# Kernel optimization log

Measured on AMD Instinct MI355X. Metric: run time of the kernel, lower is better.

## Reference

```python
import jax, jax.numpy as jnp
import numpy as np

B, P, D_MODEL = 16, 256, 1024
V, D_LLM = 1000, 4096
H, DK = 16, 64  # d_keys = d_model // n_heads


def setup_inputs() -> dict:
    key = jax.random.key(0)
    ks = jax.random.split(key, 11)
    s = lambda k, shape, fan: jax.random.normal(k, shape, jnp.float32) / np.sqrt(fan)
    return {
        "target_embedding": jax.random.normal(ks[0], (B, P, D_MODEL), jnp.float32),
        "source_embedding": jax.random.normal(ks[1], (V, D_LLM), jnp.float32),
        "value_embedding": jax.random.normal(ks[2], (V, D_LLM), jnp.float32),
        "Wq": s(ks[3], (D_MODEL, H * DK), D_MODEL),
        "bq": jnp.zeros((H * DK,), jnp.float32),
        "Wk": s(ks[4], (D_LLM, H * DK), D_LLM),
        "bk": jnp.zeros((H * DK,), jnp.float32),
        "Wv": s(ks[5], (D_LLM, H * DK), D_LLM),
        "bv": jnp.zeros((H * DK,), jnp.float32),
        "Wo": s(ks[6], (H * DK, D_LLM), H * DK),
        "bo": jnp.zeros((D_LLM,), jnp.float32),
    }


def reference(target_embedding, source_embedding, value_embedding,
              Wq, bq, Wk, bk, Wv, bv, Wo, bo):
    b, p, _ = target_embedding.shape
    v = source_embedding.shape[0]
    # projections
    Q = (target_embedding @ Wq + bq).reshape(b, p, H, DK)   # bphd
    K = (source_embedding @ Wk + bk).reshape(v, H, DK)      # vhd
    Vv = (value_embedding @ Wv + bv).reshape(v, H, DK)      # vhd
    scale = 1.0 / np.sqrt(DK)
    # NOTE: non-standard einsum — contracts over v, elementwise in d
    scores = jnp.einsum('bphd,vhd->bhpd', Q, K)             # [B,H,P,DK]
    A = jax.nn.softmax(scale * scores, axis=-1)             # softmax over head dim d
    # (dropout is identity in eval mode)
    R = jnp.einsum('bhpd,vhd->bphd', A, Vv)                 # A * sum_v V
    out = R.reshape(b, p, H * DK) @ Wo + bo                 # [B,P,D_LLM]
    return out
```

## Files before the change

### kernel.cpp

```cpp
#include <hip/hip_runtime.h>

#define BB   16
#define PP   256
#define BP   4096
#define DMODEL 1024
#define VV   1000
#define DLLM 4096
#define HH   16
#define DK   64
#define HDK  1024

using f32x4 = __attribute__((ext_vector_type(4))) float;
using s16x8 = __attribute__((ext_vector_type(8))) short;
using us8   = __attribute__((ext_vector_type(8))) unsigned short;

__device__ __forceinline__ unsigned short f2bf(float f) {
    unsigned int u = __builtin_bit_cast(unsigned int, f);
    u = (u + 0x7FFFu + ((u >> 16) & 1u)) >> 16;
    return (unsigned short)u;
}

__device__ __forceinline__ void gload_lds16(const unsigned short* g, unsigned short* lds) {
    __builtin_amdgcn_global_load_lds(
        (const __attribute__((address_space(1))) void*)g,
        (__attribute__((address_space(3))) void*)lds,
        16, 0, 0);
}

__device__ __forceinline__ void transpose_body(const float* __restrict__ src,
                                               unsigned short* __restrict__ dst,
                                               int R, int C, int bx, int by, int t,
                                               float (*tile)[33]) {
    int x = t & 7, y = t >> 3;
    int c0 = bx * 32, r0 = by * 32;
    float4 v = *reinterpret_cast<const float4*>(&src[(size_t)(r0 + y) * C + c0 + x * 4]);
    tile[y][x * 4 + 0] = v.x; tile[y][x * 4 + 1] = v.y;
    tile[y][x * 4 + 2] = v.z; tile[y][x * 4 + 3] = v.w;
    __syncthreads();
    ushort4 o = make_ushort4(f2bf(tile[x * 4 + 0][y]), f2bf(tile[x * 4 + 1][y]),
                             f2bf(tile[x * 4 + 2][y]), f2bf(tile[x * 4 + 3][y]));
    *reinterpret_cast<ushort4*>(&dst[(size_t)(c0 + y) * R + r0 + x * 4]) = o;
}

__global__ void mega1(const float* __restrict__ src0, const float* __restrict__ src1,
                      float* __restrict__ part1,
                      const float* __restrict__ target, unsigned short* __restrict__ tgt_bf,
                      const float* __restrict__ Wq, unsigned short* __restrict__ wq_t,
                      const float* __restrict__ Wo, unsigned short* __restrict__ wo_t) {
    __shared__ float tile[32][33];
    int b = blockIdx.x, t = threadIdx.x;
    if (b < 320) {
        int z = b / 160, rem = b % 160, y = rem >> 2, x = rem & 3;
        int col4 = x * 256 + t;
        const float4* src = reinterpret_cast<const float4*>(z ? src1 : src0);
        int r0 = y * 25;
        float4 acc = make_float4(0.f, 0.f, 0.f, 0.f);
        for (int r = 0; r < 25; ++r) {
            float4 v = src[(size_t)(r0 + r) * (DLLM / 4) + col4];
            acc.x += v.x; acc.y += v.y; acc.z += v.z; acc.w += v.w;
        }
        reinterpret_cast<float4*>(part1)[(size_t)(z * 40 + y) * (DLLM / 4) + col4] = acc;
    } else if (b < 320 + 2048) {
        int idx = (b - 320) * 256 + t;
        float4 v0 = reinterpret_cast<const float4*>(target)[idx * 2];
        float4 v1 = reinterpret_cast<const float4*>(target)[idx * 2 + 1];
        us8 o = { f2bf(v0.x), f2bf(v0.y), f2bf(v0.z), f2bf(v0.w),
                  f2bf(v1.x), f2bf(v1.y), f2bf(v1.z), f2bf(v1.w) };
        *reinterpret_cast<us8*>(&tgt_bf[(size_t)idx * 8]) = o;
    } else if (b < 320 + 2048 + 1024) {
        int b2 = b - 2368;
        transpose_body(Wq, wq_t, DMODEL, HDK, b2 & 31, b2 >> 5, t, tile);
    } else {
        int b2 = b - 3392;
        transpose_body(Wo, wo_t, HDK, DLLM, b2 & 127, b2 >> 7, t, tile);
    }
}

__global__ void gemv_partial2(const float* __restrict__ Wk, const float* __restrict__ Wv,
                              const float* __restrict__ part1, float* __restrict__ part2) {
    __shared__ float vec[64];
    int c     = blockIdx.x * 256 + threadIdx.x;
    int chunk = blockIdx.y;
    int z     = blockIdx.z;
    const float* W = z ? Wv : Wk;
    if (threadIdx.x < 64) {
        int r = chunk * 64 + threadIdx.x;
        float a = 0.f;
        for (int p = 0; p < 40; ++p)
            a += part1[(size_t)(z * 40 + p) * DLLM + r];
        vec[threadIdx.x] = a;
    }
    __syncthreads();
    float acc = 0.f;
    int r0 = chunk * 64;
    for (int r = 0; r < 64; ++r)
        acc += vec[r] * W[(size_t)(r0 + r) * HDK + c];
    part2[((z * 64 + chunk) * HDK) + c] = acc;
}

__global__ void gemv_reduce(const float* __restrict__ part,
                            const float* __restrict__ bk, const float* __restrict__ bv,
                            float* __restrict__ kvsum) {
    int idx = blockIdx.x * 256 + threadIdx.x;
    int z = idx >> 10, c = idx & 1023;
    float acc = 0.f;
    for (int ch = 0; ch < 64; ++ch) acc += part[(size_t)(z * 64 + ch) * HDK + c];
    acc += (float)VV * (z ? bv[c] : bk[c]);
    kvsum[idx] = acc;
}

template<int EPI, int BMt, int BNt, int WM, int WN, int BMPX, int NXBN, int BNPX>
__global__ __launch_bounds__(WM * WN * 64, 2)
void gemm_ctd3(const unsigned short* __restrict__ A, const unsigned short* __restrict__ Bt,
               float* __restrict__ C, const float* __restrict__ bias,
               const float* __restrict__ kvsum, unsigned short* __restrict__ R,
               int N, int K) {
    constexpr int WAVES = WM * WN;
    constexpr int Mw = BMt / WM;
    constexpr int M_REP = Mw / 16;
    constexpr int NA = BMt * 32 / (WAVES * 512);
    constexpr int NB = BNt * 32 / (WAVES * 512);
    constexpr int NST = NA + NB;
    static_assert(BNt / WN == 64, "wave col span must be 64");
    static_assert(NA >= 1 && NB >= 1, "staging geometry");

    __shared__ __align__(16) unsigned short Asm[3][BMt * 32];
    __shared__ __align__(16) unsigned short Bsm[3][BNt * 32];

    const int xcd = blockIdx.x & 7, l = blockIdx.x >> 3;
    const int bm = ((xcd / NXBN) * BMPX + (l % BMPX)) * BMt;
    const int bn = ((xcd % NXBN) * BNPX + (l / BMPX)) * BNt;

    const int t = threadIdx.x;
    const int w = t >> 6, lane = t & 63;
    const int wr = w / WN, wc = w % WN;
    const int l15 = lane & 15, kgrp = lane >> 4;

    size_t goffA[NA], goffB[NB];
    int ldsoA[NA], ldsoB[NB];
    {
        int s8 = lane & 7, jj = lane >> 3;
#pragma unroll
        for (int i = 0; i < NA; ++i) {
            int sr = (i * WAVES + w) * 8 + jj;
            int x = s8 ^ (sr & 7);
            goffA[i] = (size_t)(bm + sr * 2 + (x >> 2)) * K + (x & 3) * 8;
            ldsoA[i] = (i * WAVES + w) * 512;
        }
#pragma unroll
        for (int i = 0; i < NB; ++i) {
            int sr = (i * WAVES + w) * 8 + jj;
            int x = s8 ^ (sr & 7);
            goffB[i] = (size_t)(bn + sr * 2 + (x >> 2)) * K + (x & 3) * 8;
            ldsoB[i] = (i * WAVES + w) * 512;
        }
    }
    int ra[M_REP], rb[4];
#pragma unroll
    for (int m = 0; m < M_REP; ++m) {
        int r = wr * Mw + m * 16 + l15;
        int s8 = (kgrp + 4 * (r & 1)) ^ ((r >> 1) & 7);
        ra[m] = (r >> 1) * 64 + s8 * 8;
    }
#pragma unroll
    for (int n = 0; n < 4; ++n) {
        int r = wc * 64 + n * 16 + l15;
        int s8 = (kgrp + 4 * (r & 1)) ^ ((r >> 1) & 7);
        rb[n] = (r >> 1) * 64 + s8 * 8;
    }

    f32x4 acc[M_REP][4] = {};

#define STAGE(t_, b_) do { size_t k0_ = (size_t)(t_) * 32;             \
    _Pragma("unroll")                                                  \
    for (int i_ = 0; i_ < NA; ++i_)                                    \
        gload_lds16(A + goffA[i_] + k0_, &Asm[b_][ldsoA[i_]]);         \
    _Pragma("unroll")                                                  \
    for (int i_ = 0; i_ < NB; ++i_)                                    \
        gload_lds16(Bt + goffB[i_] + k0_, &Bsm[b_][ldsoB[i_]]); } while (0)

#define WAIT_NST() do {                                                 \
    if constexpr (NST == 6) asm volatile("s_waitcnt vmcnt(6)" ::: "memory"); \
    else if constexpr (NST == 4) asm volatile("s_waitcnt vmcnt(4)" ::: "memory"); \
    else if constexpr (NST == 3) asm volatile("s_waitcnt vmcnt(3)" ::: "memory"); \
    else asm volatile("s_waitcnt vmcnt(2)" ::: "memory"); } while (0)

    const int nT = K >> 5;
    STAGE(0, 0); STAGE(1, 1);
    WAIT_NST();
    __builtin_amdgcn_s_barrier();

    int cur = 0;
    for (int tk = 0; tk < nT; ++tk) {
        s16x8 af[M_REP], bfr[4];
#pragma unroll
        for (int m = 0; m < M_REP; ++m)
            af[m] = *reinterpret_cast<const s16x8*>(&Asm[cur][ra[m]]);
#pragma unroll
        for (int n = 0; n < 4; ++n)
            bfr[n] = *reinterpret_cast<const s16x8*>(&Bsm[cur][rb[n]]);
        if (tk + 2 < nT) STAGE(tk + 2, cur == 0 ? 2 : cur - 1);
        __builtin_amdgcn_s_setprio(1);
#pragma unroll
        for (int m = 0; m < M_REP; ++m)
#pragma unroll
            for (int n = 0; n < 4; ++n)
                acc[m][n] = __builtin_amdgcn_mfma_f32_16x16x32_bf16(af[m], bfr[n], acc[m][n], 0, 0, 0);
        __builtin_amdgcn_s_setprio(0);
        if (tk + 2 < nT) {
            WAIT_NST();
        } else if (tk + 1 < nT) {
            asm volatile("s_waitcnt vmcnt(0)" ::: "memory");
        }
        if (tk + 1 < nT) __builtin_amdgcn_s_barrier();
        cur = (cur == 2) ? 0 : cur + 1;
    }
#undef STAGE
#undef WAIT_NST

    if (EPI == 0) {
#pragma unroll
        for (int m = 0; m < M_REP; ++m) {
            int grow = bm + wr * Mw + m * 16 + kgrp * 4;
#pragma unroll
            for (int n = 0; n < 4; ++n) {
                int gcol = bn + wc * 64 + n * 16 + l15;
                float bb = bias[gcol];
#pragma unroll
                for (int j = 0; j < 4; ++j)
                    C[(size_t)(grow + j) * N + gcol] = acc[m][n][j] + bb;
            }
        }
    } else {
        float bqv[4], ksv[4], vsv[4];
#pragma unroll
        for (int n = 0; n < 4; ++n) {
            int col = bn + wc * 64 + n * 16 + l15;
            bqv[n] = bias[col];
            ksv[n] = kvsum[col];
            vsv[n] = kvsum[HDK + col];
        }
#pragma unroll
        for (int m = 0; m < M_REP; ++m) {
            int grow = bm + wr * Mw + m * 16 + kgrp * 4;
#pragma unroll
            for (int j = 0; j < 4; ++j) {
                float x[4];
#pragma unroll
                for (int n = 0; n < 4; ++n)
                    x[n] = 0.125f * (acc[m][n][j] + bqv[n]) * ksv[n];
                float mx = fmaxf(fmaxf(x[0], x[1]), fmaxf(x[2], x[3]));
#pragma unroll
                for (int off = 8; off; off >>= 1) mx = fmaxf(mx, __shfl_xor(mx, off));
                float e[4], s = 0.f;
#pragma unroll
                for (int n = 0; n < 4; ++n) { e[n] = __expf(x[n] - mx); s += e[n]; }
#pragma unroll
                for (int off = 8; off; off >>= 1) s += __shfl_xor(s, off);
                float inv = 1.0f / s;
#pragma unroll
                for (int n = 0; n < 4; ++n) {
                    int col = bn + wc * 64 + n * 16 + l15;
                    R[(size_t)(grow + j) * N + col] = f2bf(e[n] * inv * vsv[n]);
                }
            }
        }
    }
}

extern "C" void kernel_launch(void* const* d_in, const int* in_sizes, int n_in,
                              void* d_out, int out_size, void* d_ws, size_t ws_size,
                              hipStream_t stream) {
    const float* target = (const float*)d_in[0];
    const float* source = (const float*)d_in[1];
    const float* value  = (const float*)d_in[2];
    const float* Wq = (const float*)d_in[3];
    const float* bq = (const float*)d_in[4];
    const float* Wk = (const float*)d_in[5];
    const float* bk = (const float*)d_in[6];
    const float* Wv = (const float*)d_in[7];
    const float* bv = (const float*)d_in[8];
    const float* Wo = (const float*)d_in[9];
    const float* bo = (const float*)d_in[10];
    float* out = (float*)d_out;

    char* ws = (char*)d_ws;
    float*          part1  = (float*)(ws);
    float*          part2  = (float*)(ws + 0x180000);
    float*          kvsum  = (float*)(ws + 0x210000);
    unsigned short* tgt_bf = (unsigned short*)(ws + 0x400000);
    unsigned short* wq_t   = (unsigned short*)(ws + 0xC00000);
    unsigned short* wo_t   = (unsigned short*)(ws + 0xE00000);
    unsigned short* Rb     = (unsigned short*)(ws + 0x1600000);

    mega1<<<7488, 256, 0, stream>>>(source, value, part1, target, tgt_bf, Wq, wq_t, Wo, wo_t);

    gemv_partial2<<<dim3(4, 64, 2), 256, 0, stream>>>(Wk, Wv, part1, part2);
    gemv_reduce<<<8, 256, 0, stream>>>(part2, bk, bv, kvsum);

    gemm_ctd3<1, 64, 128, 2, 2, 16, 2, 4><<<512, 256, 0, stream>>>(
        tgt_bf, wq_t, nullptr, bq, kvsum, Rb, HDK, DMODEL);

    gemm_ctd3<0, 256, 128, 2, 2, 8, 4, 8><<<512, 256, 0, stream>>>(
        Rb, wo_t, out, bo, nullptr, nullptr, DLLM, HDK);
}
```

Before: 93.15 us.

## Restructure GEMM main loop with register double-buffered fragments and 4-stage LDS ring

The GEMM K-loop is unrolled by two and keeps two sets of register fragments, so the LDS reads for the next tile are issued before the MFMAs on the current tile. The LDS ring grows from 3 to 4 buffers, which lets the per-iteration barrier move ahead of the fragment reads. The output GEMM also switches from 256x128 to 128x128 tiles with twice as many blocks, trading more A/B reloads for more parallelism. LDS use per block rises, and this may reduce occupancy.

```diff
diff --git a/kernel.cpp b/kernel.cpp
--- a/kernel.cpp
+++ b/kernel.cpp
@@ -111,7 +111,7 @@
 
 template<int EPI, int BMt, int BNt, int WM, int WN, int BMPX, int NXBN, int BNPX>
 __global__ __launch_bounds__(WM * WN * 64, 2)
-void gemm_ctd3(const unsigned short* __restrict__ A, const unsigned short* __restrict__ Bt,
+void gemm_pipe(const unsigned short* __restrict__ A, const unsigned short* __restrict__ Bt,
                float* __restrict__ C, const float* __restrict__ bias,
                const float* __restrict__ kvsum, unsigned short* __restrict__ R,
                int N, int K) {
@@ -124,8 +124,8 @@
     static_assert(BNt / WN == 64, "wave col span must be 64");
     static_assert(NA >= 1 && NB >= 1, "staging geometry");
 
-    __shared__ __align__(16) unsigned short Asm[3][BMt * 32];
-    __shared__ __align__(16) unsigned short Bsm[3][BNt * 32];
+    __shared__ __align__(16) unsigned short Asm[4][BMt * 32];
+    __shared__ __align__(16) unsigned short Bsm[4][BNt * 32];
 
     const int xcd = blockIdx.x & 7, l = blockIdx.x >> 3;
     const int bm = ((xcd / NXBN) * BMPX + (l % BMPX)) * BMt;
@@ -184,39 +184,53 @@
     else if constexpr (NST == 4) asm volatile("s_waitcnt vmcnt(4)" ::: "memory"); \
     else if constexpr (NST == 3) asm volatile("s_waitcnt vmcnt(3)" ::: "memory"); \
     else asm volatile("s_waitcnt vmcnt(2)" ::: "memory"); } while (0)
+#define WAIT_VM0() asm volatile("s_waitcnt vmcnt(0)" ::: "memory")
+
+#define READF(fa_, fb_, buf_) do {                                      \
+    _Pragma("unroll")                                                   \
+    for (int m_ = 0; m_ < M_REP; ++m_)                                  \
+        fa_[m_] = *reinterpret_cast<const s16x8*>(&Asm[buf_][ra[m_]]);  \
+    _Pragma("unroll")                                                   \
+    for (int n_ = 0; n_ < 4; ++n_)                                      \
+        fb_[n_] = *reinterpret_cast<const s16x8*>(&Bsm[buf_][rb[n_]]); } while (0)
+
+#define MFMAS(fa_, fb_) do {                                            \
+    __builtin_amdgcn_s_setprio(1);                                      \
+    _Pragma("unroll")                                                   \
+    for (int m_ = 0; m_ < M_REP; ++m_)                                  \
+        _Pragma("unroll")                                               \
+        for (int n_ = 0; n_ < 4; ++n_)                                  \
+            acc[m_][n_] = __builtin_amdgcn_mfma_f32_16x16x32_bf16(      \
+                fa_[m_], fb_[n_], acc[m_][n_], 0, 0, 0);                \
+    __builtin_amdgcn_s_setprio(0); } while (0)
 
     const int nT = K >> 5;
+    s16x8 fa0[M_REP], fb0[4], fa1[M_REP], fb1[4];
+
     STAGE(0, 0); STAGE(1, 1);
     WAIT_NST();
     __builtin_amdgcn_s_barrier();
-
-    int cur = 0;
-    for (int tk = 0; tk < nT; ++tk) {
-        s16x8 af[M_REP], bfr[4];
-#pragma unroll
-        for (int m = 0; m < M_REP; ++m)
-            af[m] = *reinterpret_cast<const s16x8*>(&Asm[cur][ra[m]]);
-#pragma unroll
-        for (int n = 0; n < 4; ++n)
-            bfr[n] = *reinterpret_cast<const s16x8*>(&Bsm[cur][rb[n]]);
-        if (tk + 2 < nT) STAGE(tk + 2, cur == 0 ? 2 : cur - 1);
-        __builtin_amdgcn_s_setprio(1);
-#pragma unroll
-        for (int m = 0; m < M_REP; ++m)
-#pragma unroll
-            for (int n = 0; n < 4; ++n)
-                acc[m][n] = __builtin_amdgcn_mfma_f32_16x16x32_bf16(af[m], bfr[n], acc[m][n], 0, 0, 0);
-        __builtin_amdgcn_s_setprio(0);
+    READF(fa0, fb0, 0);
+
+    for (int tk = 0; tk < nT; tk += 2) {
+        if (tk + 2 < nT) { STAGE(tk + 2, (tk + 2) & 3); WAIT_NST(); }
+        else             { WAIT_VM0(); }
+        __builtin_amdgcn_s_barrier();
+        READF(fa1, fb1, (tk + 1) & 3);
+        MFMAS(fa0, fb0);
         if (tk + 2 < nT) {
-            WAIT_NST();
-        } else if (tk + 1 < nT) {
-            asm volatile("s_waitcnt vmcnt(0)" ::: "memory");
-        }
-        if (tk + 1 < nT) __builtin_amdgcn_s_barrier();
-        cur = (cur == 2) ? 0 : cur + 1;
+            if (tk + 3 < nT) { STAGE(tk + 3, (tk + 3) & 3); WAIT_NST(); }
+            else             { WAIT_VM0(); }
+            __builtin_amdgcn_s_barrier();
+            READF(fa0, fb0, (tk + 2) & 3);
+        }
+        MFMAS(fa1, fb1);
     }
 #undef STAGE
 #undef WAIT_NST
+#undef WAIT_VM0
+#undef READF
+#undef MFMAS
 
     if (EPI == 0) {
 #pragma unroll
@@ -298,9 +312,9 @@
     gemv_partial2<<<dim3(4, 64, 2), 256, 0, stream>>>(Wk, Wv, part1, part2);
     gemv_reduce<<<8, 256, 0, stream>>>(part2, bk, bv, kvsum);
 
-    gemm_ctd3<1, 64, 128, 2, 2, 16, 2, 4><<<512, 256, 0, stream>>>(
+    gemm_pipe<1, 64, 128, 2, 2, 16, 2, 4><<<512, 256, 0, stream>>>(
         tgt_bf, wq_t, nullptr, bq, kvsum, Rb, HDK, DMODEL);
 
-    gemm_ctd3<0, 256, 128, 2, 2, 8, 4, 8><<<512, 256, 0, stream>>>(
+    gemm_pipe<0, 128, 128, 2, 2, 16, 4, 8><<<1024, 256, 0, stream>>>(
         Rb, wo_t, out, bo, nullptr, nullptr, DLLM, HDK);
 }
```

New measurement: 102.1 us. 1.1x slower.

## Make GEMM kernels persistent over two M tiles with half the grid

Applied to the files above, without the earlier changes.

Both GEMM kernels now launch 256 blocks instead of 512. Each block loops over two M tiles offset by half the rows and reuses its precomputed addressing and B-column assignment. The tile-to-XCD mapping parameters change so that coverage stays complete. This is meant to cut block launch and tail overhead and to fit one wave of blocks on the device. The cost is a serialized prologue and epilogue per tile, with no overlap between tiles, and possibly lower latency hiding.

```diff
diff --git a/kernel.cpp b/kernel.cpp
--- a/kernel.cpp
+++ b/kernel.cpp
@@ -109,12 +109,12 @@
     kvsum[idx] = acc;
 }
 
-template<int EPI, int BMt, int BNt, int WM, int WN, int BMPX, int NXBN, int BNPX>
+template<int EPI, int BMt, int BNt, int WM, int WN, int BMPX, int NXBN, int BNPX, int NTILES>
 __global__ __launch_bounds__(WM * WN * 64, 2)
-void gemm_ctd3(const unsigned short* __restrict__ A, const unsigned short* __restrict__ Bt,
+void gemm_pers(const unsigned short* __restrict__ A, const unsigned short* __restrict__ Bt,
                float* __restrict__ C, const float* __restrict__ bias,
                const float* __restrict__ kvsum, unsigned short* __restrict__ R,
-               int N, int K) {
+               int N, int K, int Mhalf) {
     constexpr int WAVES = WM * WN;
     constexpr int Mw = BMt / WM;
     constexpr int M_REP = Mw / 16;
@@ -128,8 +128,8 @@
     __shared__ __align__(16) unsigned short Bsm[3][BNt * 32];
 
     const int xcd = blockIdx.x & 7, l = blockIdx.x >> 3;
-    const int bm = ((xcd / NXBN) * BMPX + (l % BMPX)) * BMt;
-    const int bn = ((xcd % NXBN) * BNPX + (l / BMPX)) * BNt;
+    const int bm0 = ((xcd / NXBN) * BMPX + (l % BMPX)) * BMt;
+    const int bn  = ((xcd % NXBN) * BNPX + (l / BMPX)) * BNt;
 
     const int t = threadIdx.x;
     const int w = t >> 6, lane = t & 63;
@@ -144,7 +144,7 @@
         for (int i = 0; i < NA; ++i) {
             int sr = (i * WAVES + w) * 8 + jj;
             int x = s8 ^ (sr & 7);
-            goffA[i] = (size_t)(bm + sr * 2 + (x >> 2)) * K + (x & 3) * 8;
+            goffA[i] = (size_t)(bm0 + sr * 2 + (x >> 2)) * K + (x & 3) * 8;
             ldsoA[i] = (i * WAVES + w) * 512;
         }
 #pragma unroll
@@ -169,12 +169,10 @@
         rb[n] = (r >> 1) * 64 + s8 * 8;
     }
 
-    f32x4 acc[M_REP][4] = {};
-
-#define STAGE(t_, b_) do { size_t k0_ = (size_t)(t_) * 32;             \
+#define STAGE(t_, b_, At_) do { size_t k0_ = (size_t)(t_) * 32;        \
     _Pragma("unroll")                                                  \
     for (int i_ = 0; i_ < NA; ++i_)                                    \
-        gload_lds16(A + goffA[i_] + k0_, &Asm[b_][ldsoA[i_]]);         \
+        gload_lds16(At_ + goffA[i_] + k0_, &Asm[b_][ldsoA[i_]]);       \
     _Pragma("unroll")                                                  \
     for (int i_ = 0; i_ < NB; ++i_)                                    \
         gload_lds16(Bt + goffB[i_] + k0_, &Bsm[b_][ldsoB[i_]]); } while (0)
@@ -184,88 +182,100 @@
     else if constexpr (NST == 4) asm volatile("s_waitcnt vmcnt(4)" ::: "memory"); \
     else if constexpr (NST == 3) asm volatile("s_waitcnt vmcnt(3)" ::: "memory"); \
     else asm volatile("s_waitcnt vmcnt(2)" ::: "memory"); } while (0)
+#define WAIT_VM0() asm volatile("s_waitcnt vmcnt(0)" ::: "memory")
 
     const int nT = K >> 5;
-    STAGE(0, 0); STAGE(1, 1);
-    WAIT_NST();
-    __builtin_amdgcn_s_barrier();
-
-    int cur = 0;
-    for (int tk = 0; tk < nT; ++tk) {
-        s16x8 af[M_REP], bfr[4];
-#pragma unroll
-        for (int m = 0; m < M_REP; ++m)
-            af[m] = *reinterpret_cast<const s16x8*>(&Asm[cur][ra[m]]);
-#pragma unroll
-        for (int n = 0; n < 4; ++n)
-            bfr[n] = *reinterpret_cast<const s16x8*>(&Bsm[cur][rb[n]]);
-        if (tk + 2 < nT) STAGE(tk + 2, cur == 0 ? 2 : cur - 1);
-        __builtin_amdgcn_s_setprio(1);
-#pragma unroll
-        for (int m = 0; m < M_REP; ++m)
+
+    for (int tt = 0; tt < NTILES; ++tt) {
+        const int bmx = bm0 + tt * Mhalf;
+        const unsigned short* At = A + (size_t)tt * Mhalf * K;
+
+        f32x4 acc[M_REP][4] = {};
+
+        if (tt > 0) __builtin_amdgcn_s_barrier();
+        STAGE(0, 0, At); STAGE(1, 1, At);
+        if (tt == 0) { WAIT_NST(); }
+        else         { WAIT_VM0(); }
+        __builtin_amdgcn_s_barrier();
+
+        int cur = 0;
+        for (int tk = 0; tk < nT; ++tk) {
+            s16x8 af[M_REP], bfr[4];
+#pragma unroll
+            for (int m = 0; m < M_REP; ++m)
+                af[m] = *reinterpret_cast<const s16x8*>(&Asm[cur][ra[m]]);
 #pragma unroll
             for (int n = 0; n < 4; ++n)
-                acc[m][n] = __builtin_amdgcn_mfma_f32_16x16x32_bf16(af[m], bfr[n], acc[m][n], 0, 0, 0);
-        __builtin_amdgcn_s_setprio(0);
-        if (tk + 2 < nT) {
-            WAIT_NST();
-        } else if (tk + 1 < nT) {
-            asm volatile("s_waitcnt vmcnt(0)" ::: "memory");
-        }
-        if (tk + 1 < nT) __builtin_amdgcn_s_barrier();
-        cur = (cur == 2) ? 0 : cur + 1;
+                bfr[n] = *reinterpret_cast<const s16x8*>(&Bsm[cur][rb[n]]);
+            if (tk + 2 < nT) STAGE(tk + 2, cur == 0 ? 2 : cur - 1, At);
+            __builtin_amdgcn_s_setprio(1);
+#pragma unroll
+            for (int m = 0; m < M_REP; ++m)
+#pragma unroll
+                for (int n = 0; n < 4; ++n)
+                    acc[m][n] = __builtin_amdgcn_mfma_f32_16x16x32_bf16(af[m], bfr[n], acc[m][n], 0, 0, 0);
+            __builtin_amdgcn_s_setprio(0);
+            if (tk + 2 < nT) {
+                WAIT_NST();
+            } else if (tk + 1 < nT) {
+                WAIT_VM0();
+            }
+            if (tk + 1 < nT) __builtin_amdgcn_s_barrier();
+            cur = (cur == 2) ? 0 : cur + 1;
+        }
+
+        if (EPI == 0) {
+#pragma unroll
+            for (int m = 0; m < M_REP; ++m) {
+                int grow = bmx + wr * Mw + m * 16 + kgrp * 4;
+#pragma unroll
+                for (int n = 0; n < 4; ++n) {
+                    int gcol = bn + wc * 64 + n * 16 + l15;
+                    float bb = bias[gcol];
+#pragma unroll
+                    for (int j = 0; j < 4; ++j)
+                        C[(size_t)(grow + j) * N + gcol] = acc[m][n][j] + bb;
+                }
+            }
+        } else {
+            float bqv[4], ksv[4], vsv[4];
+#pragma unroll
+            for (int n = 0; n < 4; ++n) {
+                int col = bn + wc * 64 + n * 16 + l15;
+                bqv[n] = bias[col];
+                ksv[n] = kvsum[col];
+                vsv[n] = kvsum[HDK + col];
+            }
+#pragma unroll
+            for (int m = 0; m < M_REP; ++m) {
+                int grow = bmx + wr * Mw + m * 16 + kgrp * 4;
+#pragma unroll
+                for (int j = 0; j < 4; ++j) {
+                    float x[4];
+#pragma unroll
+                    for (int n = 0; n < 4; ++n)
+                        x[n] = 0.125f * (acc[m][n][j] + bqv[n]) * ksv[n];
+                    float mx = fmaxf(fmaxf(x[0], x[1]), fmaxf(x[2], x[3]));
+#pragma unroll
+                    for (int off = 8; off; off >>= 1) mx = fmaxf(mx, __shfl_xor(mx, off));
+                    float e[4], s = 0.f;
+#pragma unroll
+                    for (int n = 0; n < 4; ++n) { e[n] = __expf(x[n] - mx); s += e[n]; }
+#pragma unroll
+                    for (int off = 8; off; off >>= 1) s += __shfl_xor(s, off);
+                    float inv = 1.0f / s;
+#pragma unroll
+                    for (int n = 0; n < 4; ++n) {
+                        int col = bn + wc * 64 + n * 16 + l15;
+                        R[(size_t)(grow + j) * N + col] = f2bf(e[n] * inv * vsv[n]);
+                    }
+                }
+            }
+        }
     }
 #undef STAGE
 #undef WAIT_NST
-
-    if (EPI == 0) {
-#pragma unroll
-        for (int m = 0; m < M_REP; ++m) {
-            int grow = bm + wr * Mw + m * 16 + kgrp * 4;
-#pragma unroll
-            for (int n = 0; n < 4; ++n) {
-                int gcol = bn + wc * 64 + n * 16 + l15;
-                float bb = bias[gcol];
-#pragma unroll
-                for (int j = 0; j < 4; ++j)
-                    C[(size_t)(grow + j) * N + gcol] = acc[m][n][j] + bb;
-            }
-        }
-    } else {
-        float bqv[4], ksv[4], vsv[4];
-#pragma unroll
-        for (int n = 0; n < 4; ++n) {
-            int col = bn + wc * 64 + n * 16 + l15;
-            bqv[n] = bias[col];
-            ksv[n] = kvsum[col];
-            vsv[n] = kvsum[HDK + col];
-        }
-#pragma unroll
-        for (int m = 0; m < M_REP; ++m) {
-            int grow = bm + wr * Mw + m * 16 + kgrp * 4;
-#pragma unroll
-            for (int j = 0; j < 4; ++j) {
-                float x[4];
-#pragma unroll
-                for (int n = 0; n < 4; ++n)
-                    x[n] = 0.125f * (acc[m][n][j] + bqv[n]) * ksv[n];
-                float mx = fmaxf(fmaxf(x[0], x[1]), fmaxf(x[2], x[3]));
-#pragma unroll
-                for (int off = 8; off; off >>= 1) mx = fmaxf(mx, __shfl_xor(mx, off));
-                float e[4], s = 0.f;
-#pragma unroll
-                for (int n = 0; n < 4; ++n) { e[n] = __expf(x[n] - mx); s += e[n]; }
-#pragma unroll
-                for (int off = 8; off; off >>= 1) s += __shfl_xor(s, off);
-                float inv = 1.0f / s;
-#pragma unroll
-                for (int n = 0; n < 4; ++n) {
-                    int col = bn + wc * 64 + n * 16 + l15;
-                    R[(size_t)(grow + j) * N + col] = f2bf(e[n] * inv * vsv[n]);
-                }
-            }
-        }
-    }
+#undef WAIT_VM0
 }
 
 extern "C" void kernel_launch(void* const* d_in, const int* in_sizes, int n_in,
@@ -298,9 +308,9 @@
     gemv_partial2<<<dim3(4, 64, 2), 256, 0, stream>>>(Wk, Wv, part1, part2);
     gemv_reduce<<<8, 256, 0, stream>>>(part2, bk, bv, kvsum);
 
-    gemm_ctd3<1, 64, 128, 2, 2, 16, 2, 4><<<512, 256, 0, stream>>>(
-        tgt_bf, wq_t, nullptr, bq, kvsum, Rb, HDK, DMODEL);
-
-    gemm_ctd3<0, 256, 128, 2, 2, 8, 4, 8><<<512, 256, 0, stream>>>(
-        Rb, wo_t, out, bo, nullptr, nullptr, DLLM, HDK);
-}
+    gemm_pers<1, 64, 128, 2, 2, 16, 4, 2, 2><<<256, 256, 0, stream>>>(
+        tgt_bf, wq_t, nullptr, bq, kvsum, Rb, HDK, DMODEL, 2048);
+
+    gemm_pers<0, 256, 128, 2, 2, 4, 4, 8, 2><<<256, 256, 0, stream>>>(
+        Rb, wo_t, out, bo, nullptr, nullptr, DLLM, HDK, 2048);
+}
```

Measured after the change: 113.0 us. +21.3%, slower.

## Replace output GEMM with single-wave 128x128 tile kernel using register double-buffering

Applied to the files above, without the earlier changes.

The final Wo projection GEMM moves from the 4-wave 256x128 block kernel to a new one-wavefront-per-block kernel. Each wave computes a 128x128 tile with 64 accumulators, a two-stage LDS ring and ping-pong A-fragment registers. Explicit vmcnt/lgkmcnt waits and sched_barriers interleave loads with MFMAs. This removes block-wide barriers and aims for more MFMA work per LDS read, but uses many VGPRs, one wave per block, and 1024 blocks of low occupancy.

```diff
diff --git a/kernel.cpp b/kernel.cpp
--- a/kernel.cpp
+++ b/kernel.cpp
@@ -26,6 +26,10 @@
         (__attribute__((address_space(3))) void*)lds,
         16, 0, 0);
 }
+
+#define WAITVM(n_) asm volatile("s_waitcnt vmcnt(%0)" :: "n"(n_) : "memory")
+#define WAITLG0()  asm volatile("s_waitcnt lgkmcnt(0)" ::: "memory")
+#define SBAR0()    __builtin_amdgcn_sched_barrier(0)
 
 __device__ __forceinline__ void transpose_body(const float* __restrict__ src,
                                                unsigned short* __restrict__ dst,
@@ -122,7 +126,6 @@
     constexpr int NB = BNt * 32 / (WAVES * 512);
     constexpr int NST = NA + NB;
     static_assert(BNt / WN == 64, "wave col span must be 64");
-    static_assert(NA >= 1 && NB >= 1, "staging geometry");
 
     __shared__ __align__(16) unsigned short Asm[3][BMt * 32];
     __shared__ __align__(16) unsigned short Bsm[3][BNt * 32];
@@ -171,7 +174,7 @@
 
     f32x4 acc[M_REP][4] = {};
 
-#define STAGE(t_, b_) do { size_t k0_ = (size_t)(t_) * 32;             \
+#define STG(t_, b_) do { size_t k0_ = (size_t)(t_) * 32;               \
     _Pragma("unroll")                                                  \
     for (int i_ = 0; i_ < NA; ++i_)                                    \
         gload_lds16(A + goffA[i_] + k0_, &Asm[b_][ldsoA[i_]]);         \
@@ -179,15 +182,9 @@
     for (int i_ = 0; i_ < NB; ++i_)                                    \
         gload_lds16(Bt + goffB[i_] + k0_, &Bsm[b_][ldsoB[i_]]); } while (0)
 
-#define WAIT_NST() do {                                                 \
-    if constexpr (NST == 6) asm volatile("s_waitcnt vmcnt(6)" ::: "memory"); \
-    else if constexpr (NST == 4) asm volatile("s_waitcnt vmcnt(4)" ::: "memory"); \
-    else if constexpr (NST == 3) asm volatile("s_waitcnt vmcnt(3)" ::: "memory"); \
-    else asm volatile("s_waitcnt vmcnt(2)" ::: "memory"); } while (0)
-
     const int nT = K >> 5;
-    STAGE(0, 0); STAGE(1, 1);
-    WAIT_NST();
+    STG(0, 0); STG(1, 1);
+    WAITVM(NST);
     __builtin_amdgcn_s_barrier();
 
     int cur = 0;
@@ -199,7 +196,7 @@
 #pragma unroll
         for (int n = 0; n < 4; ++n)
             bfr[n] = *reinterpret_cast<const s16x8*>(&Bsm[cur][rb[n]]);
-        if (tk + 2 < nT) STAGE(tk + 2, cur == 0 ? 2 : cur - 1);
+        if (tk + 2 < nT) STG(tk + 2, cur == 0 ? 2 : cur - 1);
         __builtin_amdgcn_s_setprio(1);
 #pragma unroll
         for (int m = 0; m < M_REP; ++m)
@@ -207,63 +204,140 @@
             for (int n = 0; n < 4; ++n)
                 acc[m][n] = __builtin_amdgcn_mfma_f32_16x16x32_bf16(af[m], bfr[n], acc[m][n], 0, 0, 0);
         __builtin_amdgcn_s_setprio(0);
-        if (tk + 2 < nT) {
-            WAIT_NST();
-        } else if (tk + 1 < nT) {
-            asm volatile("s_waitcnt vmcnt(0)" ::: "memory");
-        }
+        if (tk + 2 < nT)      WAITVM(NST);
+        else if (tk + 1 < nT) WAITVM(0);
         if (tk + 1 < nT) __builtin_amdgcn_s_barrier();
         cur = (cur == 2) ? 0 : cur + 1;
     }
+#undef STG
+
+    float bqv[4], ksv[4], vsv[4];
+#pragma unroll
+    for (int n = 0; n < 4; ++n) {
+        int col = bn + wc * 64 + n * 16 + l15;
+        bqv[n] = bias[col];
+        ksv[n] = kvsum[col];
+        vsv[n] = kvsum[HDK + col];
+    }
+#pragma unroll
+    for (int m = 0; m < M_REP; ++m) {
+        int grow = bm + wr * Mw + m * 16 + kgrp * 4;
+#pragma unroll
+        for (int j = 0; j < 4; ++j) {
+            float x[4];
+#pragma unroll
+            for (int n = 0; n < 4; ++n)
+                x[n] = 0.125f * (acc[m][n][j] + bqv[n]) * ksv[n];
+            float mx = fmaxf(fmaxf(x[0], x[1]), fmaxf(x[2], x[3]));
+#pragma unroll
+            for (int off = 8; off; off >>= 1) mx = fmaxf(mx, __shfl_xor(mx, off));
+            float e[4], s = 0.f;
+#pragma unroll
+            for (int n = 0; n < 4; ++n) { e[n] = __expf(x[n] - mx); s += e[n]; }
+#pragma unroll
+            for (int off = 8; off; off >>= 1) s += __shfl_xor(s, off);
+            float inv = 1.0f / s;
+#pragma unroll
+            for (int n = 0; n < 4; ++n) {
+                int col = bn + wc * 64 + n * 16 + l15;
+                R[(size_t)(grow + j) * N + col] = f2bf(e[n] * inv * vsv[n]);
+            }
+        }
+    }
+}
+
+template<int BM, int BN, int K, int NXBN, int BMPX, int BNPX>
+__global__ __launch_bounds__(64, 1)
+void gemm_wave(const unsigned short* __restrict__ A, const unsigned short* __restrict__ Bt,
+               float* __restrict__ C, const float* __restrict__ bias, int N) {
+    constexpr int M_REP = BM / 16, N_REP = BN / 16;
+    constexpr int NLA = BM / 16, NLB = BN / 16;
+    constexpr int NST = NLA + NLB;
+    constexpr int AW = BM * 32;
+    constexpr int nT = K / 32;
+    static_assert(nT % 2 == 0 && nT >= 4, "K-tiling");
+    __shared__ __align__(16) unsigned short lds[2][AW + BN * 32];
+
+    const int xcd = blockIdx.x & 7, l = blockIdx.x >> 3;
+    const int bm = ((xcd / NXBN) * BMPX + (l % BMPX)) * BM;
+    const int bn = ((xcd % NXBN) * BNPX + (l / BMPX)) * BN;
+
+    const int lane = threadIdx.x;
+    const int l15 = lane & 15, kgrp = lane >> 4;
+
+    const int s8 = lane & 7, jj = lane >> 3;
+    const int xs = s8 ^ jj;
+    const int srow = jj * 2 + (xs >> 2);
+    const int scol = (xs & 3) * 8;
+    const unsigned short* gA0 = A + (size_t)(bm + srow) * K + scol;
+    const unsigned short* gB0 = Bt + (size_t)(bn + srow) * K + scol;
+
+    const int roff = (l15 >> 1) * 64 + (((kgrp + 4 * (l15 & 1)) ^ ((l15 >> 1) & 7)) * 8);
+
+    f32x4 acc[M_REP][N_REP] = {};
+    s16x8 fa0[M_REP], fa1[M_REP], fb[N_REP];
+
+#define STAGE(tk_, b_) do {                                            \
+    const unsigned short* ga_ = gA0 + (size_t)(tk_) * 32;              \
+    unsigned short* la_ = &lds[b_][0];                                 \
+    _Pragma("unroll 1")                                                \
+    for (int i_ = 0; i_ < NLA; ++i_) {                                 \
+        gload_lds16(ga_, la_); ga_ += (size_t)16 * K; la_ += 512; }    \
+    const unsigned short* gb_ = gB0 + (size_t)(tk_) * 32;              \
+    unsigned short* lb_ = &lds[b_][AW];                                \
+    _Pragma("unroll 1")                                                \
+    for (int i_ = 0; i_ < NLB; ++i_) {                                 \
+        gload_lds16(gb_, lb_); gb_ += (size_t)16 * K; lb_ += 512; } } while (0)
+
+#define READF_A(fa_, b_) do { _Pragma("unroll")                        \
+    for (int m_ = 0; m_ < M_REP; ++m_)                                 \
+        fa_[m_] = *reinterpret_cast<const s16x8*>(&lds[b_][m_ * 512 + roff]); } while (0)
+#define READF_B(b_) do { _Pragma("unroll")                             \
+    for (int n_ = 0; n_ < N_REP; ++n_)                                 \
+        fb[n_] = *reinterpret_cast<const s16x8*>(&lds[b_][AW + n_ * 512 + roff]); } while (0)
+#define MFMAS(fa_) do { _Pragma("unroll")                              \
+    for (int m_ = 0; m_ < M_REP; ++m_)                                 \
+        _Pragma("unroll")                                              \
+        for (int n_ = 0; n_ < N_REP; ++n_)                             \
+            acc[m_][n_] = __builtin_amdgcn_mfma_f32_16x16x32_bf16(     \
+                fa_[m_], fb[n_], acc[m_][n_], 0, 0, 0); } while (0)
+
+    STAGE(0, 0); STAGE(1, 1);
+    WAITVM(NST); SBAR0();
+    READF_A(fa0, 0); READF_B(0);
+    WAITLG0(); SBAR0();
+
+    for (int tk = 0; tk < nT; tk += 2) {
+        if (tk + 2 < nT) { STAGE(tk + 2, 0); WAITVM(NST); }
+        else             { WAITVM(0); }
+        SBAR0();
+        READF_A(fa1, 1);
+        MFMAS(fa0);
+        READF_B(1);
+        WAITLG0(); SBAR0();
+        if (tk + 3 < nT)      { STAGE(tk + 3, 1); WAITVM(NST); }
+        else if (tk + 2 < nT) { WAITVM(0); }
+        SBAR0();
+        if (tk + 2 < nT) READF_A(fa0, 0);
+        MFMAS(fa1);
+        if (tk + 2 < nT) READF_B(0);
+        WAITLG0(); SBAR0();
+    }
 #undef STAGE
-#undef WAIT_NST
-
-    if (EPI == 0) {
-#pragma unroll
-        for (int m = 0; m < M_REP; ++m) {
-            int grow = bm + wr * Mw + m * 16 + kgrp * 4;
-#pragma unroll
-            for (int n = 0; n < 4; ++n) {
-                int gcol = bn + wc * 64 + n * 16 + l15;
-                float bb = bias[gcol];
-#pragma unroll
-                for (int j = 0; j < 4; ++j)
-                    C[(size_t)(grow + j) * N + gcol] = acc[m][n][j] + bb;
-            }
-        }
-    } else {
-        float bqv[4], ksv[4], vsv[4];
-#pragma unroll
-        for (int n = 0; n < 4; ++n) {
-            int col = bn + wc * 64 + n * 16 + l15;
-            bqv[n] = bias[col];
-            ksv[n] = kvsum[col];
-            vsv[n] = kvsum[HDK + col];
-        }
-#pragma unroll
-        for (int m = 0; m < M_REP; ++m) {
-            int grow = bm + wr * Mw + m * 16 + kgrp * 4;
-#pragma unroll
-            for (int j = 0; j < 4; ++j) {
-                float x[4];
-#pragma unroll
-                for (int n = 0; n < 4; ++n)
-                    x[n] = 0.125f * (acc[m][n][j] + bqv[n]) * ksv[n];
-                float mx = fmaxf(fmaxf(x[0], x[1]), fmaxf(x[2], x[3]));
-#pragma unroll
-                for (int off = 8; off; off >>= 1) mx = fmaxf(mx, __shfl_xor(mx, off));
-                float e[4], s = 0.f;
-#pragma unroll
-                for (int n = 0; n < 4; ++n) { e[n] = __expf(x[n] - mx); s += e[n]; }
-#pragma unroll
-                for (int off = 8; off; off >>= 1) s += __shfl_xor(s, off);
-                float inv = 1.0f / s;
-#pragma unroll
-                for (int n = 0; n < 4; ++n) {
-                    int col = bn + wc * 64 + n * 16 + l15;
-                    R[(size_t)(grow + j) * N + col] = f2bf(e[n] * inv * vsv[n]);
-                }
-            }
+#undef READF_A
+#undef READF_B
+#undef MFMAS
+
+#pragma unroll
+    for (int m = 0; m < M_REP; ++m) {
+        int grow = bm + m * 16 + kgrp * 4;
+#pragma unroll
+        for (int n = 0; n < N_REP; ++n) {
+            int gcol = bn + n * 16 + l15;
+            float bb = bias[gcol];
+#pragma unroll
+            for (int j = 0; j < 4; ++j)
+                C[(size_t)(grow + j) * N + gcol] = acc[m][n][j] + bb;
         }
     }
 }
@@ -301,6 +375,6 @@
     gemm_ctd3<1, 64, 128, 2, 2, 16, 2, 4><<<512, 256, 0, stream>>>(
         tgt_bf, wq_t, nullptr, bq, kvsum, Rb, HDK, DMODEL);
 
-    gemm_ctd3<0, 256, 128, 2, 2, 8, 4, 8><<<512, 256, 0, stream>>>(
-        Rb, wo_t, out, bo, nullptr, nullptr, DLLM, HDK);
-}
+    gemm_wave<128, 128, 1024, 4, 16, 8><<<1024, 64, 0, stream>>>(
+        Rb, wo_t, out, bo, DLLM);
+}
```

New measurement: 136.8 us. 1.47x slower.
